# Kernel optimization log

Measured on AMD Instinct MI355X. Metric: run time of the kernel, lower is better.

The kernel has to match this reference:

```python
import jax, jax.numpy as jnp
import numpy as np

B, N, D, H = 4, 2048, 64, 8

def setup_inputs() -> dict:
    key = jax.random.key(0)
    ks = jax.random.split(key, 6)
    s = 0.05
    return {
        "x":  jax.random.normal(ks[0], (B, N, D), dtype=jnp.float32),
        "Wq": jax.random.normal(ks[1], (D, D * H), dtype=jnp.float32) * s,
        "Wk": jax.random.normal(ks[2], (D, D * H), dtype=jnp.float32) * s,
        "Wv": jax.random.normal(ks[3], (D, D * H), dtype=jnp.float32) * s,
        "Wu": jax.random.normal(ks[4], (D * H, D), dtype=jnp.float32) * s,
        "bu": jnp.zeros((D,), dtype=jnp.float32),
    }

def reference(x, Wq, Wk, Wv, Wu, bu):
    b, n, d = x.shape
    h = Wq.shape[1] // d
    # projections: each head has full width d (per the original module)
    q = (x @ Wq).reshape(b, n, h, d).transpose(0, 2, 1, 3)  # [b,h,n,d]
    k = (x @ Wk).reshape(b, n, h, d).transpose(0, 2, 1, 3)
    v = (x @ Wv).reshape(b, n, h, d).transpose(0, 2, 1, 3)
    scores = jnp.einsum('bhnd,bhmd->bhnm', q, k) / jnp.sqrt(jnp.float32(d))
    w = jax.nn.softmax(scores, axis=-1)
    y = jnp.einsum('bhnm,bhmd->bhnd', w, v)          # [b,h,n,d]
    y = y.transpose(0, 2, 1, 3).reshape(b, n, h * d)  # [b,n,h*d]
    return y @ Wu + bu
```

## Files before the change

### kernel.cpp

```cpp
#include <hip/hip_runtime.h>
#include <hip/hip_bf16.h>

#define BB 4
#define NN 2048
#define DD 64
#define HH 8
#define DHH 512

typedef __bf16 bf16_t;
typedef __bf16 bf16x8 __attribute__((ext_vector_type(8)));
typedef __bf16 bf16x4 __attribute__((ext_vector_type(4)));
typedef float f32x4 __attribute__((ext_vector_type(4)));
typedef long long i64;
typedef i64 i64x2 __attribute__((ext_vector_type(2)));
typedef _Float16 f16_t;
typedef _Float16 f16x4 __attribute__((ext_vector_type(4)));
typedef __fp16 h16x2 __attribute__((ext_vector_type(2)));

__device__ __forceinline__ void dma16(const void* g, void* l) {
    __builtin_amdgcn_global_load_lds(
        (const __attribute__((address_space(1))) unsigned int*)g,
        (__attribute__((address_space(3))) unsigned int*)l,
        16, 0, 0);
}

#define MFMA   __builtin_amdgcn_mfma_f32_16x16x32_bf16
#define MFMA8  __builtin_amdgcn_mfma_f32_16x16x32_fp8_fp8
#define MFMA16F __builtin_amdgcn_mfma_f32_16x16x16f16

#define QSCALE 0.18033688011112042f


__global__ __launch_bounds__(256) void prep(
    const float* __restrict__ Wq, const float* __restrict__ Wk,
    const float* __restrict__ Wv, const float* __restrict__ Wu,
    bf16_t* __restrict__ Wqt, bf16_t* __restrict__ Wkt,
    bf16_t* __restrict__ Wvt, bf16_t* __restrict__ Wut)
{
    const int bid = blockIdx.x, tid = threadIdx.x;
    if (bid < 48) {
        const int m = bid >> 4, slice = bid & 15;
        const float* src = (m == 0) ? Wq : (m == 1) ? Wk : Wv;
        bf16_t* dst = (m == 0) ? Wqt : (m == 1) ? Wkt : Wvt;
        const float scale = (m == 0) ? QSCALE : 1.0f;
        const int dc = slice * 32 + (tid >> 3);
        const int kbase = (tid & 7) * 8;
        bf16x8 p;
        #pragma unroll
        for (int j = 0; j < 8; ++j)
            p[j] = (bf16_t)(src[(size_t)(kbase + j) * 512 + dc] * scale);
        *(bf16x8*)(dst + dc * 64 + kbase) = p;
    } else {
        const int kq = (bid - 48) * 32;
        const int dc = tid >> 2, sub = (tid & 3) * 8;
        bf16x8 p;
        #pragma unroll
        for (int j = 0; j < 8; ++j)
            p[j] = (bf16_t)Wu[(size_t)(kq + sub + j) * 64 + dc];
        *(bf16x8*)(Wut + dc * 512 + kq + sub) = p;
    }
}

__global__ __launch_bounds__(256) void qkv_mfma(
    const float* __restrict__ x, const bf16_t* __restrict__ Wqt,
    const bf16_t* __restrict__ Wkt, const bf16_t* __restrict__ Wvt,
    char* __restrict__ q8, char* __restrict__ k8, f16_t* __restrict__ vt)
{
    const int n0   = blockIdx.x * 64;
    const int h    = blockIdx.y;
    const int tid  = threadIdx.x;
    const int w    = tid >> 6;
    const int lane = tid & 63;
    const int quad = lane >> 4;
    const int c    = lane & 15;
    const int cq   = c & 7;
    const int l8   = lane >> 3;
    const int lg   = (lane & 7) ^ l8;
    const int lo   = l8 * 128 + lg * 16;
    const int sw0  = ((quad    ) ^ cq) * 16;
    const int sw1  = ((quad + 4) ^ cq) * 16;
    const int w2048 = w * 2048;

    __shared__ __align__(16) float  xs[64 * 64];
    __shared__ __align__(16) bf16_t Wqs[64 * 64], Wks[64 * 64], Wvs[64 * 64];

    {
        const int rloc = lane >> 4;
        const int s    = lane & 15;
        #pragma unroll
        for (int j = 0; j < 4; ++j) {
            int chunk = w * 4 + j;
            int r7 = (chunk * 4 + rloc) & 7;
            const char* src = (const char*)(x + (size_t)(n0 + chunk * 4 + rloc) * 64)
                            + ((s & 8) | ((s & 7) ^ r7)) * 16;
            dma16(src, (char*)xs + chunk * 1024);
        }
    }
    const char* qg = (const char*)Wqt + (size_t)h * 8192;
    const char* kg = (const char*)Wkt + (size_t)h * 8192;
    const char* vg = (const char*)Wvt + (size_t)h * 8192;
    dma16(qg + w2048 + lo,        (char*)Wqs + w2048);
    dma16(qg + w2048 + 1024 + lo, (char*)Wqs + w2048 + 1024);
    dma16(kg + w2048 + lo,        (char*)Wks + w2048);
    dma16(kg + w2048 + 1024 + lo, (char*)Wks + w2048 + 1024);
    dma16(vg + w2048 + lo,        (char*)Wvs + w2048);
    dma16(vg + w2048 + 1024 + lo, (char*)Wvs + w2048 + 1024);
    __syncthreads();

    auto xfrag = [&](int row, int kk) -> bf16x8 {
        const char* rbase = (const char*)xs + row * 256;
        int g0 = kk * 8 + ((quad * 2    ) ^ cq);
        int g1 = kk * 8 + ((quad * 2 + 1) ^ cq);
        f32x4 a = *(const f32x4*)(rbase + g0 * 16);
        f32x4 b = *(const f32x4*)(rbase + g1 * 16);
        bf16x8 r;
        r[0] = (bf16_t)a[0]; r[1] = (bf16_t)a[1]; r[2] = (bf16_t)a[2]; r[3] = (bf16_t)a[3];
        r[4] = (bf16_t)b[0]; r[5] = (bf16_t)b[1]; r[6] = (bf16_t)b[2]; r[7] = (bf16_t)b[3];
        return r;
    };

    bf16x8 xf0 = xfrag(w * 16 + c, 0);
    bf16x8 xf1 = xfrag(w * 16 + c, 1);

    const int gr = n0 + w * 16 + c;
    const int bb = gr >> 11, nn = gr & 2047;
    char* qrow_g = q8 + (((size_t)bb * HH + h) * NN + nn) * 64;
    char* krow_g = k8 + (((size_t)bb * HH + h) * NN + nn) * 64;
    const int nsw = (nn & 3) ^ ((nn >> 2) & 3);

    #pragma unroll
    for (int mb = 0; mb < 4; ++mb) {
        const char* aq = (const char*)Wqs + (mb * 16 + c) * 128;
        const char* ak = (const char*)Wks + (mb * 16 + c) * 128;
        f32x4 accq = (f32x4){0.f, 0.f, 0.f, 0.f};
        f32x4 acck = (f32x4){0.f, 0.f, 0.f, 0.f};
        accq = MFMA(*(const bf16x8*)(aq + sw0), xf0, accq, 0, 0, 0);
        accq = MFMA(*(const bf16x8*)(aq + sw1), xf1, accq, 0, 0, 0);
        acck = MFMA(*(const bf16x8*)(ak + sw0), xf0, acck, 0, 0, 0);
        acck = MFMA(*(const bf16x8*)(ak + sw1), xf1, acck, 0, 0, 0);
        int g2  = (mb * 2 + (quad >> 1)) & 3;
        int off = ((quad & 1) * 4) + ((mb >> 1) * 8) + ((g2 ^ nsw) * 16);
        int pq = __builtin_amdgcn_cvt_pk_fp8_f32(accq[0], accq[1], 0, false);
        pq     = __builtin_amdgcn_cvt_pk_fp8_f32(accq[2], accq[3], pq, true);
        int pk = __builtin_amdgcn_cvt_pk_fp8_f32(acck[0], acck[1], 0, false);
        pk     = __builtin_amdgcn_cvt_pk_fp8_f32(acck[2], acck[3], pk, true);
        *(int*)(qrow_g + off) = pq;
        *(int*)(krow_g + off) = pk;
    }

    const char* wvrow = (const char*)Wvs + (w * 16 + c) * 128;
    bf16x8 vf0 = *(const bf16x8*)(wvrow + sw0);
    bf16x8 vf1 = *(const bf16x8*)(wvrow + sw1);

    const int bb2 = n0 >> 11;
    f16_t* vtb = vt + ((size_t)bb2 * HH + h) * (size_t)(DD * NN)
               + (size_t)((n0 & 2047) >> 4) * 1024 + quad * 256 + (w * 16 + c) * 4;

    #pragma unroll
    for (int nb = 0; nb < 4; ++nb) {
        f32x4 acc = (f32x4){0.f, 0.f, 0.f, 0.f};
        acc = MFMA(xfrag(nb * 16 + c, 0), vf0, acc, 0, 0, 0);
        acc = MFMA(xfrag(nb * 16 + c, 1), vf1, acc, 0, 0, 0);
        f16x4 p = { (f16_t)acc[0], (f16_t)acc[1], (f16_t)acc[2], (f16_t)acc[3] };
        *(f16x4*)(vtb + nb * 1024) = p;
    }
}

__global__ __launch_bounds__(256, 3) void flash_attn(
    const char* __restrict__ q8, const char* __restrict__ k8,
    const f16_t* __restrict__ vt, bf16_t* __restrict__ y)
{
    const int h    = blockIdx.x;
    const int n0   = blockIdx.y * 64;
    const int b    = blockIdx.z;
    const int tid  = threadIdx.x;
    const int w    = tid >> 6;
    const int lane = tid & 63;
    const int quad = lane >> 4;
    const int c    = lane & 15;
    const int ksw  = (quad ^ (c & 3) ^ ((c >> 2) & 3)) * 16;

    __shared__ __align__(16) char SM[49152];

    const size_t bh = (size_t)(b * HH + h);
    const char* qp = q8 + bh * (size_t)(NN * 64);
    const char* kp = k8 + bh * (size_t)(NN * 64);
    const char* vp = (const char*)(vt + bh * (size_t)(DD * NN));

    i64x2 qf[4];
    #pragma unroll
    for (int cb = 0; cb < 4; ++cb)
        qf[cb] = *(const i64x2*)(qp + (size_t)(n0 + cb * 16 + c) * 64 + ksw);

    const char* kdma = kp + w * 1024 + lane * 16;
    const char* vdma = vp + w * 2048 + lane * 16;

    const int kro = w * 2048 + c * 64 + ksw;
    const int vro = 8192 + w * 4096 + quad * 512 + c * 8;

    f32x4 lsum4[4];
    f32x4 o[4][4];
    #pragma unroll
    for (int cb = 0; cb < 4; ++cb) lsum4[cb] = (f32x4){0.f, 0.f, 0.f, 0.f};
    #pragma unroll
    for (int db = 0; db < 4; ++db)
        #pragma unroll
        for (int cb = 0; cb < 4; ++cb) o[db][cb] = (f32x4){0.f, 0.f, 0.f, 0.f};

    #define STAGE2(p, buf) do {                                               \
        char* B_ = SM + (buf) * 24576;                                        \
        const size_t t0_ = (size_t)(2 * (p));                                 \
        dma16(kdma + t0_ * 4096,         B_ + w * 2048);                      \
        dma16(kdma + t0_ * 4096 + 4096,  B_ + w * 2048 + 1024);               \
        dma16(vdma + t0_ * 8192,         B_ + 8192 + w * 4096);               \
        dma16(vdma + t0_ * 8192 + 1024,  B_ + 8192 + w * 4096 + 1024);        \
        dma16(vdma + t0_ * 8192 + 8192,  B_ + 8192 + w * 4096 + 2048);        \
        dma16(vdma + t0_ * 8192 + 9216,  B_ + 8192 + w * 4096 + 3072);        \
    } while (0)

    #define BODY2(buf, hf) do {                                               \
        const char* kb_b = SM + (buf) * 24576;                                \
        i64x2 kf_ = *(const i64x2*)(kb_b + kro + (hf) * 1024);                \
        f16x4 vf_[4];                                                         \
        _Pragma("unroll")                                                     \
        for (int db = 0; db < 4; ++db)                                        \
            vf_[db] = *(const f16x4*)(kb_b + vro + (hf) * 2048 + db * 128);   \
        _Pragma("unroll")                                                     \
        for (int cb = 0; cb < 4; ++cb) {                                      \
            f32x4 s_ = (f32x4){0.f, 0.f, 0.f, 0.f};                           \
            s_ = MFMA8(kf_.x, qf[cb].x, s_, 0, 0, 0);                         \
            s_ = MFMA8(kf_.y, qf[cb].y, s_, 0, 0, 0);                         \
            float p0_ = __builtin_amdgcn_exp2f(s_[0]);                        \
            float p1_ = __builtin_amdgcn_exp2f(s_[1]);                        \
            float p2_ = __builtin_amdgcn_exp2f(s_[2]);                        \
            float p3_ = __builtin_amdgcn_exp2f(s_[3]);                        \
            lsum4[cb] += (f32x4){p0_, p1_, p2_, p3_};                         \
            h16x2 ab_ = __builtin_amdgcn_cvt_pkrtz(p0_, p1_);                 \
            h16x2 cd_ = __builtin_amdgcn_cvt_pkrtz(p2_, p3_);                 \
            f16x4 pf_;                                                        \
            __builtin_memcpy(&pf_, &ab_, 4);                                  \
            __builtin_memcpy((char*)&pf_ + 4, &cd_, 4);                       \
            _Pragma("unroll")                                                 \
            for (int db = 0; db < 4; ++db)                                    \
                o[db][cb] = MFMA16F(vf_[db], pf_, o[db][cb], 0, 0, 0);        \
        }                                                                     \
    } while (0)

    STAGE2(0, 0);
    asm volatile("s_waitcnt vmcnt(0)" ::: "memory");
    __builtin_amdgcn_sched_barrier(0);
    STAGE2(1, 1);

    #pragma unroll 1
    for (int p = 0; p < 16; ++p) {
        BODY2(p & 1, 0);
        BODY2(p & 1, 1);
        if (p < 15) {
            __builtin_amdgcn_sched_barrier(0);
            if (p < 14) {
                STAGE2(p + 2, p & 1);
                asm volatile("s_waitcnt vmcnt(6)" ::: "memory");
            } else {
                asm volatile("s_waitcnt vmcnt(0)" ::: "memory");
            }
            __builtin_amdgcn_sched_barrier(0);
        }
    }

    #undef STAGE2
    #undef BODY2

    float lsum[4];
    #pragma unroll
    for (int cb = 0; cb < 4; ++cb)
        lsum[cb] = (lsum4[cb][0] + lsum4[cb][1]) + (lsum4[cb][2] + lsum4[cb][3]);

    __syncthreads();

    char*  Ob = SM;
    float* Lb = (float*)(SM + 16384);

    #pragma unroll
    for (int cb = 0; cb < 4; ++cb) {
        lsum[cb] += __shfl_xor(lsum[cb], 16, 64);
        lsum[cb] += __shfl_xor(lsum[cb], 32, 64);
    }
    if (quad == 0) {
        #pragma unroll
        for (int cb = 0; cb < 4; ++cb)
            Lb[(w * 4 + cb) * 16 + c] = lsum[cb];
    }

    #pragma unroll
    for (int ww = 0; ww < 4; ++ww) {
        if (w == ww) {
            #pragma unroll
            for (int db = 0; db < 4; ++db) {
                #pragma unroll
                for (int cb = 0; cb < 4; ++cb) {
                    char* p = Ob + (size_t)(((db * 4 + cb) * 4 + quad) * 16 + c) * 16;
                    f32x4 v = o[db][cb];
                    if (ww > 0) v += *(const f32x4*)p;
                    *(f32x4*)p = v;
                }
            }
        }
        __syncthreads();
    }

    {
        const int n_loc = tid & 63;
        const int dq    = tid >> 6;
        const int qcb   = n_loc >> 4;
        const int cc    = n_loc & 15;
        float l = Lb[(0 * 4 + qcb) * 16 + cc] + Lb[(1 * 4 + qcb) * 16 + cc]
                + Lb[(2 * 4 + qcb) * 16 + cc] + Lb[(3 * 4 + qcb) * 16 + cc];
        float inv = 1.0f / l;
        float vals[16];
        #pragma unroll
        for (int q2 = 0; q2 < 4; ++q2) {
            f32x4 v = *(const f32x4*)(Ob
                    + (size_t)(((dq * 4 + qcb) * 4 + q2) * 16 + cc) * 16);
            vals[q2 * 4 + 0] = v[0]; vals[q2 * 4 + 1] = v[1];
            vals[q2 * 4 + 2] = v[2]; vals[q2 * 4 + 3] = v[3];
        }
        bf16x8 o0, o1;
        #pragma unroll
        for (int j = 0; j < 8; ++j) {
            o0[j] = (bf16_t)(vals[j] * inv);
            o1[j] = (bf16_t)(vals[8 + j] * inv);
        }
        bf16_t* yrow = y + bh * (size_t)(NN * DD) + (size_t)(n0 + n_loc) * DD + dq * 16;
        *(bf16x8*)(yrow)     = o0;
        *(bf16x8*)(yrow + 8) = o1;
    }
}

__global__ __launch_bounds__(256) void out_proj(
    const bf16_t* __restrict__ y,
    const bf16_t* __restrict__ Wut,
    const float* __restrict__ bu, float* __restrict__ out)
{
    const int rt   = blockIdx.x >> 1;
    const int dh   = blockIdx.x & 1;
    const int row0 = rt * 32;
    const int b    = row0 >> 11;
    const int nn0  = row0 & 2047;
    const int tid  = threadIdx.x;
    const int w    = tid >> 6;
    const int lane = tid & 63;
    const int quad = lane >> 4;
    const int c    = lane & 15;
    const int cq   = c & 7;

    __shared__ __align__(16) bf16_t ys[32 * 512];

    {
        const int hsel = lane >> 3;
        const int g7   = lane & 7;
        #pragma unroll
        for (int rr = 0; rr < 8; ++rr) {
            int row = w * 8 + rr;
            const char* src = (const char*)y
                + (((size_t)b * HH + hsel) * NN + nn0 + row) * 128
                + ((g7 ^ (row & 7)) * 16);
            dma16(src, (char*)ys + row * 1024);
        }
    }
    __syncthreads();

    const int rows16 = (w >> 1) * 16;
    const int mb     = dh * 2 + (w & 1);
    const char* yrow = (const char*)ys + (rows16 + c) * 1024;

    f32x4 acc = (f32x4){0.f, 0.f, 0.f, 0.f};
    #pragma unroll
    for (int kk = 0; kk < 16; ++kk) {
        int g = kk * 4 + quad;
        bf16x8 bfrag = *(const bf16x8*)(yrow + (((g & ~7) | ((g & 7) ^ cq)) * 16));
        bf16x8 afrag = *(const bf16x8*)((const char*)Wut
                        + (size_t)(mb * 16 + c) * 1024 + kk * 64 + quad * 16);
        acc = MFMA(afrag, bfrag, acc, 0, 0, 0);
    }

    float4 bb = *(const float4*)(bu + mb * 16 + quad * 4);
    float4 res = { acc[0] + bb.x, acc[1] + bb.y, acc[2] + bb.z, acc[3] + bb.w };
    float* op = out + (size_t)(row0 + rows16 + c) * DD + mb * 16 + quad * 4;
    *(float4*)op = res;
}

extern "C" void kernel_launch(void* const* d_in, const int* in_sizes, int n_in,
                              void* d_out, int out_size, void* d_ws, size_t ws_size,
                              hipStream_t stream) {
    const float* x  = (const float*)d_in[0];
    const float* Wq = (const float*)d_in[1];
    const float* Wk = (const float*)d_in[2];
    const float* Wv = (const float*)d_in[3];
    const float* Wu = (const float*)d_in[4];
    const float* bu = (const float*)d_in[5];
    float* out = (float*)d_out;

    const size_t SEG8 = (size_t)BB * HH * NN * 64;
    const size_t SEG  = SEG8 * 2;
    char* ws = (char*)d_ws;
    char*   q8  = ws;
    char*   k8  = ws + SEG8;
    f16_t*  vt  = (f16_t*)(ws + 2 * SEG8);
    bf16_t* y   = (bf16_t*)(ws + 2 * SEG8 + SEG);
    bf16_t* Wqt = (bf16_t*)(ws + 2 * SEG8 + 2 * SEG);
    bf16_t* Wkt = (bf16_t*)(ws + 2 * SEG8 + 2 * SEG + (1 << 16));
    bf16_t* Wvt = (bf16_t*)(ws + 2 * SEG8 + 2 * SEG + 2 * (1 << 16));
    bf16_t* Wut = (bf16_t*)(ws + 2 * SEG8 + 2 * SEG + 3 * (1 << 16));

    prep<<<dim3(64), dim3(256), 0, stream>>>(Wq, Wk, Wv, Wu, Wqt, Wkt, Wvt, Wut);
    qkv_mfma<<<dim3(128, 8), dim3(256), 0, stream>>>(x, Wqt, Wkt, Wvt, q8, k8, vt);
    flash_attn<<<dim3(HH, NN / 64, BB), dim3(256), 0, stream>>>(q8, k8, vt, y);
    out_proj<<<dim3(512), dim3(256), 0, stream>>>(y, Wut, bu, out);
}
```

Measured before the change: 126.4 us.

## Deepen K/V prefetch pipeline to five single-tile LDS buffers

Replaces the double-buffered two-tile staging with a five-slot ring of single 64-key tiles, keeping four tiles in flight ahead of compute. Each iteration waits only for the oldest outstanding tile, so more global-load latency is hidden. LDS per block grows from 48KB to 60KB and launch bounds drop from three to two blocks per SIMD, which trades occupancy for pipeline depth. The final stage re-fetches tile 31 redundantly to keep the wait count uniform.

```diff
diff --git a/kernel.cpp b/kernel.cpp
--- a/kernel.cpp
+++ b/kernel.cpp
@@ -166,7 +166,7 @@
     }
 }
 
-__global__ __launch_bounds__(256, 3) void flash_attn(
+__global__ __launch_bounds__(256, 2) void flash_attn(
     const char* __restrict__ q8, const char* __restrict__ k8,
     const f16_t* __restrict__ vt, bf16_t* __restrict__ y)
 {
@@ -180,7 +180,7 @@
     const int c    = lane & 15;
     const int ksw  = (quad ^ (c & 3) ^ ((c >> 2) & 3)) * 16;
 
-    __shared__ __align__(16) char SM[49152];
+    __shared__ __align__(16) char SM[61440];
 
     const size_t bh = (size_t)(b * HH + h);
     const char* qp = q8 + bh * (size_t)(NN * 64);
@@ -195,8 +195,8 @@
     const char* kdma = kp + w * 1024 + lane * 16;
     const char* vdma = vp + w * 2048 + lane * 16;
 
-    const int kro = w * 2048 + c * 64 + ksw;
-    const int vro = 8192 + w * 4096 + quad * 512 + c * 8;
+    const int kro = w * 1024 + c * 64 + ksw;
+    const int vro = 4096 + w * 2048 + quad * 512 + c * 8;
 
     f32x4 lsum4[4];
     f32x4 o[4][4];
@@ -207,24 +207,20 @@
         #pragma unroll
         for (int cb = 0; cb < 4; ++cb) o[db][cb] = (f32x4){0.f, 0.f, 0.f, 0.f};
 
-    #define STAGE2(p, buf) do {                                               \
-        char* B_ = SM + (buf) * 24576;                                        \
-        const size_t t0_ = (size_t)(2 * (p));                                 \
-        dma16(kdma + t0_ * 4096,         B_ + w * 2048);                      \
-        dma16(kdma + t0_ * 4096 + 4096,  B_ + w * 2048 + 1024);               \
-        dma16(vdma + t0_ * 8192,         B_ + 8192 + w * 4096);               \
-        dma16(vdma + t0_ * 8192 + 1024,  B_ + 8192 + w * 4096 + 1024);        \
-        dma16(vdma + t0_ * 8192 + 8192,  B_ + 8192 + w * 4096 + 2048);        \
-        dma16(vdma + t0_ * 8192 + 9216,  B_ + 8192 + w * 4096 + 3072);        \
+    #define STAGE1(t, buf) do {                                               \
+        char* B_ = SM + (buf) * 12288;                                        \
+        dma16(kdma + (size_t)(t) * 4096,        B_ + w * 1024);               \
+        dma16(vdma + (size_t)(t) * 8192,        B_ + 4096 + w * 2048);        \
+        dma16(vdma + (size_t)(t) * 8192 + 1024, B_ + 4096 + w * 2048 + 1024); \
     } while (0)
 
-    #define BODY2(buf, hf) do {                                               \
-        const char* kb_b = SM + (buf) * 24576;                                \
-        i64x2 kf_ = *(const i64x2*)(kb_b + kro + (hf) * 1024);                \
+    #define BODY1(buf) do {                                                   \
+        const char* kb_b = SM + (buf) * 12288;                                \
+        i64x2 kf_ = *(const i64x2*)(kb_b + kro);                              \
         f16x4 vf_[4];                                                         \
         _Pragma("unroll")                                                     \
         for (int db = 0; db < 4; ++db)                                        \
-            vf_[db] = *(const f16x4*)(kb_b + vro + (hf) * 2048 + db * 128);   \
+            vf_[db] = *(const f16x4*)(kb_b + vro + db * 128);                 \
         _Pragma("unroll")                                                     \
         for (int cb = 0; cb < 4; ++cb) {                                      \
             f32x4 s_ = (f32x4){0.f, 0.f, 0.f, 0.f};                           \
@@ -246,29 +242,28 @@
         }                                                                     \
     } while (0)
 
-    STAGE2(0, 0);
+    STAGE1(0, 0);
+    STAGE1(1, 1);
+    STAGE1(2, 2);
+    STAGE1(3, 3);
+    asm volatile("s_waitcnt vmcnt(9)" ::: "memory");
+    __builtin_amdgcn_sched_barrier(0);
+
+    #pragma unroll 1
+    for (int t = 0; t < 32; ++t) {
+        BODY1(t % 5);
+        if (t < 31) {
+            __builtin_amdgcn_sched_barrier(0);
+            const int ts = (t + 4 < 32) ? (t + 4) : 31;
+            STAGE1(ts, (t + 4) % 5);
+            asm volatile("s_waitcnt vmcnt(9)" ::: "memory");
+            __builtin_amdgcn_sched_barrier(0);
+        }
+    }
     asm volatile("s_waitcnt vmcnt(0)" ::: "memory");
-    __builtin_amdgcn_sched_barrier(0);
-    STAGE2(1, 1);
-
-    #pragma unroll 1
-    for (int p = 0; p < 16; ++p) {
-        BODY2(p & 1, 0);
-        BODY2(p & 1, 1);
-        if (p < 15) {
-            __builtin_amdgcn_sched_barrier(0);
-            if (p < 14) {
-                STAGE2(p + 2, p & 1);
-                asm volatile("s_waitcnt vmcnt(6)" ::: "memory");
-            } else {
-                asm volatile("s_waitcnt vmcnt(0)" ::: "memory");
-            }
-            __builtin_amdgcn_sched_barrier(0);
-        }
-    }
-
-    #undef STAGE2
-    #undef BODY2
+
+    #undef STAGE1
+    #undef BODY1
 
     float lsum[4];
     #pragma unroll
```

Result: slower. 130.7 us (+3.5%).

## Fuse output projection into flash attention epilogue with atomic accumulation

Applied to the files above, without the earlier changes.

Removes the separate out_proj kernel and the bf16 y intermediate. Each attention block now multiplies its normalized per-head output tile by that head's slice of Wu with MFMA and atomically adds the result into the fp32 output. Head 0 contributes the bias, and the prep kernel zero-fills the output beforehand. This saves a launch and a global round trip for y, but adds contention from eight heads doing fp32 atomics on the same output elements, and the summation order is no longer deterministic.

```diff
diff --git a/kernel.cpp b/kernel.cpp
--- a/kernel.cpp
+++ b/kernel.cpp
@@ -35,9 +35,17 @@
     const float* __restrict__ Wq, const float* __restrict__ Wk,
     const float* __restrict__ Wv, const float* __restrict__ Wu,
     bf16_t* __restrict__ Wqt, bf16_t* __restrict__ Wkt,
-    bf16_t* __restrict__ Wvt, bf16_t* __restrict__ Wut)
+    bf16_t* __restrict__ Wvt, bf16_t* __restrict__ Wut,
+    float* __restrict__ out)
 {
     const int bid = blockIdx.x, tid = threadIdx.x;
+    {
+        float4 z = {0.f, 0.f, 0.f, 0.f};
+        float* op = out + (size_t)bid * 8192 + tid * 4;
+        #pragma unroll
+        for (int i = 0; i < 8; ++i)
+            *(float4*)(op + i * 1024) = z;
+    }
     if (bid < 48) {
         const int m = bid >> 4, slice = bid & 15;
         const float* src = (m == 0) ? Wq : (m == 1) ? Wk : Wv;
@@ -168,7 +176,8 @@
 
 __global__ __launch_bounds__(256, 3) void flash_attn(
     const char* __restrict__ q8, const char* __restrict__ k8,
-    const f16_t* __restrict__ vt, bf16_t* __restrict__ y)
+    const f16_t* __restrict__ vt, const bf16_t* __restrict__ Wut,
+    const float* __restrict__ bu, float* __restrict__ out)
 {
     const int h    = blockIdx.x;
     const int n0   = blockIdx.y * 64;
@@ -309,84 +318,52 @@
     }
 
     {
-        const int n_loc = tid & 63;
-        const int dq    = tid >> 6;
-        const int qcb   = n_loc >> 4;
-        const int cc    = n_loc & 15;
-        float l = Lb[(0 * 4 + qcb) * 16 + cc] + Lb[(1 * 4 + qcb) * 16 + cc]
-                + Lb[(2 * 4 + qcb) * 16 + cc] + Lb[(3 * 4 + qcb) * 16 + cc];
+        float l = Lb[(0 * 4 + w) * 16 + c] + Lb[(1 * 4 + w) * 16 + c]
+                + Lb[(2 * 4 + w) * 16 + c] + Lb[(3 * 4 + w) * 16 + c];
         float inv = 1.0f / l;
-        float vals[16];
-        #pragma unroll
-        for (int q2 = 0; q2 < 4; ++q2) {
-            f32x4 v = *(const f32x4*)(Ob
-                    + (size_t)(((dq * 4 + qcb) * 4 + q2) * 16 + cc) * 16);
-            vals[q2 * 4 + 0] = v[0]; vals[q2 * 4 + 1] = v[1];
-            vals[q2 * 4 + 2] = v[2]; vals[q2 * 4 + 3] = v[3];
-        }
-        bf16x8 o0, o1;
-        #pragma unroll
-        for (int j = 0; j < 8; ++j) {
-            o0[j] = (bf16_t)(vals[j] * inv);
-            o1[j] = (bf16_t)(vals[8 + j] * inv);
-        }
-        bf16_t* yrow = y + bh * (size_t)(NN * DD) + (size_t)(n0 + n_loc) * DD + dq * 16;
-        *(bf16x8*)(yrow)     = o0;
-        *(bf16x8*)(yrow + 8) = o1;
-    }
-}
-
-__global__ __launch_bounds__(256) void out_proj(
-    const bf16_t* __restrict__ y,
-    const bf16_t* __restrict__ Wut,
-    const float* __restrict__ bu, float* __restrict__ out)
-{
-    const int rt   = blockIdx.x >> 1;
-    const int dh   = blockIdx.x & 1;
-    const int row0 = rt * 32;
-    const int b    = row0 >> 11;
-    const int nn0  = row0 & 2047;
-    const int tid  = threadIdx.x;
-    const int w    = tid >> 6;
-    const int lane = tid & 63;
-    const int quad = lane >> 4;
-    const int c    = lane & 15;
-    const int cq   = c & 7;
-
-    __shared__ __align__(16) bf16_t ys[32 * 512];
-
-    {
-        const int hsel = lane >> 3;
-        const int g7   = lane & 7;
-        #pragma unroll
-        for (int rr = 0; rr < 8; ++rr) {
-            int row = w * 8 + rr;
-            const char* src = (const char*)y
-                + (((size_t)b * HH + hsel) * NN + nn0 + row) * 128
-                + ((g7 ^ (row & 7)) * 16);
-            dma16(src, (char*)ys + row * 1024);
-        }
-    }
-    __syncthreads();
-
-    const int rows16 = (w >> 1) * 16;
-    const int mb     = dh * 2 + (w & 1);
-    const char* yrow = (const char*)ys + (rows16 + c) * 1024;
-
-    f32x4 acc = (f32x4){0.f, 0.f, 0.f, 0.f};
-    #pragma unroll
-    for (int kk = 0; kk < 16; ++kk) {
-        int g = kk * 4 + quad;
-        bf16x8 bfrag = *(const bf16x8*)(yrow + (((g & ~7) | ((g & 7) ^ cq)) * 16));
-        bf16x8 afrag = *(const bf16x8*)((const char*)Wut
-                        + (size_t)(mb * 16 + c) * 1024 + kk * 64 + quad * 16);
-        acc = MFMA(afrag, bfrag, acc, 0, 0, 0);
-    }
-
-    float4 bb = *(const float4*)(bu + mb * 16 + quad * 4);
-    float4 res = { acc[0] + bb.x, acc[1] + bb.y, acc[2] + bb.z, acc[3] + bb.w };
-    float* op = out + (size_t)(row0 + rows16 + c) * DD + mb * 16 + quad * 4;
-    *(float4*)op = res;
+
+        f32x4 acc[4];
+        #pragma unroll
+        for (int mb = 0; mb < 4; ++mb) {
+            if (h == 0) {
+                float4 bb4 = *(const float4*)(bu + mb * 16 + quad * 4);
+                acc[mb] = (f32x4){bb4.x, bb4.y, bb4.z, bb4.w};
+            } else {
+                acc[mb] = (f32x4){0.f, 0.f, 0.f, 0.f};
+            }
+        }
+
+        #pragma unroll
+        for (int kk = 0; kk < 2; ++kk) {
+            const int db = kk * 2 + (quad >> 1);
+            const int q0 = (quad & 1) * 2;
+            f32x4 blo = *(const f32x4*)(Ob
+                      + (size_t)(((db * 4 + w) * 4 + q0    ) * 16 + c) * 16);
+            f32x4 bhi = *(const f32x4*)(Ob
+                      + (size_t)(((db * 4 + w) * 4 + q0 + 1) * 16 + c) * 16);
+            bf16x8 bf;
+            bf[0] = (bf16_t)(blo[0] * inv); bf[1] = (bf16_t)(blo[1] * inv);
+            bf[2] = (bf16_t)(blo[2] * inv); bf[3] = (bf16_t)(blo[3] * inv);
+            bf[4] = (bf16_t)(bhi[0] * inv); bf[5] = (bf16_t)(bhi[1] * inv);
+            bf[6] = (bf16_t)(bhi[2] * inv); bf[7] = (bf16_t)(bhi[3] * inv);
+            #pragma unroll
+            for (int mb = 0; mb < 4; ++mb) {
+                bf16x8 af = *(const bf16x8*)((const char*)Wut
+                          + (size_t)(mb * 16 + c) * 1024 + h * 128
+                          + kk * 64 + quad * 16);
+                acc[mb] = MFMA(af, bf, acc[mb], 0, 0, 0);
+            }
+        }
+
+        float* orow = out + ((size_t)b * NN + n0 + w * 16 + c) * DD + quad * 4;
+        #pragma unroll
+        for (int mb = 0; mb < 4; ++mb) {
+            atomicAdd(orow + mb * 16 + 0, acc[mb][0]);
+            atomicAdd(orow + mb * 16 + 1, acc[mb][1]);
+            atomicAdd(orow + mb * 16 + 2, acc[mb][2]);
+            atomicAdd(orow + mb * 16 + 3, acc[mb][3]);
+        }
+    }
 }
 
 extern "C" void kernel_launch(void* const* d_in, const int* in_sizes, int n_in,
@@ -406,14 +383,12 @@
     char*   q8  = ws;
     char*   k8  = ws + SEG8;
     f16_t*  vt  = (f16_t*)(ws + 2 * SEG8);
-    bf16_t* y   = (bf16_t*)(ws + 2 * SEG8 + SEG);
     bf16_t* Wqt = (bf16_t*)(ws + 2 * SEG8 + 2 * SEG);
     bf16_t* Wkt = (bf16_t*)(ws + 2 * SEG8 + 2 * SEG + (1 << 16));
     bf16_t* Wvt = (bf16_t*)(ws + 2 * SEG8 + 2 * SEG + 2 * (1 << 16));
     bf16_t* Wut = (bf16_t*)(ws + 2 * SEG8 + 2 * SEG + 3 * (1 << 16));
 
-    prep<<<dim3(64), dim3(256), 0, stream>>>(Wq, Wk, Wv, Wu, Wqt, Wkt, Wvt, Wut);
+    prep<<<dim3(64), dim3(256), 0, stream>>>(Wq, Wk, Wv, Wu, Wqt, Wkt, Wvt, Wut, out);
     qkv_mfma<<<dim3(128, 8), dim3(256), 0, stream>>>(x, Wqt, Wkt, Wvt, q8, k8, vt);
-    flash_attn<<<dim3(HH, NN / 64, BB), dim3(256), 0, stream>>>(q8, k8, vt, y);
-    out_proj<<<dim3(512), dim3(256), 0, stream>>>(y, Wut, bu, out);
-}
+    flash_attn<<<dim3(HH, NN / 64, BB), dim3(256), 0, stream>>>(q8, k8, vt, Wut, bu, out);
+}
```

Result: slower. 150.4 us (+19.0%).

## Fold weight prep kernel into QKV projection, staging fp32 weights directly

Applied to the files above, without the earlier changes.

Removes the separate prep launch. The QKV kernel now DMAs the fp32 Wq/Wk/Wv head slices straight into LDS and converts them to bf16 (with the Q scale applied) while building MFMA fragments. The Wu transpose is done by a subset of blocks at the end of the QKV kernel. This saves one kernel launch and one global round-trip for the converted weights. In exchange it adds extra LDS traffic, strided scalar LDS reads, a second staging pass with two more barriers for Wv, and redundant conversion work repeated in every block.

```diff
diff --git a/kernel.cpp b/kernel.cpp
--- a/kernel.cpp
+++ b/kernel.cpp
@@ -9,7 +9,6 @@
 
 typedef __bf16 bf16_t;
 typedef __bf16 bf16x8 __attribute__((ext_vector_type(8)));
-typedef __bf16 bf16x4 __attribute__((ext_vector_type(4)));
 typedef float f32x4 __attribute__((ext_vector_type(4)));
 typedef long long i64;
 typedef i64 i64x2 __attribute__((ext_vector_type(2)));
@@ -31,40 +30,12 @@
 #define QSCALE 0.18033688011112042f
 
 
-__global__ __launch_bounds__(256) void prep(
+__global__ __launch_bounds__(256) void qkv_mfma(
+    const float* __restrict__ x,
     const float* __restrict__ Wq, const float* __restrict__ Wk,
     const float* __restrict__ Wv, const float* __restrict__ Wu,
-    bf16_t* __restrict__ Wqt, bf16_t* __restrict__ Wkt,
-    bf16_t* __restrict__ Wvt, bf16_t* __restrict__ Wut)
-{
-    const int bid = blockIdx.x, tid = threadIdx.x;
-    if (bid < 48) {
-        const int m = bid >> 4, slice = bid & 15;
-        const float* src = (m == 0) ? Wq : (m == 1) ? Wk : Wv;
-        bf16_t* dst = (m == 0) ? Wqt : (m == 1) ? Wkt : Wvt;
-        const float scale = (m == 0) ? QSCALE : 1.0f;
-        const int dc = slice * 32 + (tid >> 3);
-        const int kbase = (tid & 7) * 8;
-        bf16x8 p;
-        #pragma unroll
-        for (int j = 0; j < 8; ++j)
-            p[j] = (bf16_t)(src[(size_t)(kbase + j) * 512 + dc] * scale);
-        *(bf16x8*)(dst + dc * 64 + kbase) = p;
-    } else {
-        const int kq = (bid - 48) * 32;
-        const int dc = tid >> 2, sub = (tid & 3) * 8;
-        bf16x8 p;
-        #pragma unroll
-        for (int j = 0; j < 8; ++j)
-            p[j] = (bf16_t)Wu[(size_t)(kq + sub + j) * 64 + dc];
-        *(bf16x8*)(Wut + dc * 512 + kq + sub) = p;
-    }
-}
-
-__global__ __launch_bounds__(256) void qkv_mfma(
-    const float* __restrict__ x, const bf16_t* __restrict__ Wqt,
-    const bf16_t* __restrict__ Wkt, const bf16_t* __restrict__ Wvt,
-    char* __restrict__ q8, char* __restrict__ k8, f16_t* __restrict__ vt)
+    char* __restrict__ q8, char* __restrict__ k8, f16_t* __restrict__ vt,
+    bf16_t* __restrict__ Wut)
 {
     const int n0   = blockIdx.x * 64;
     const int h    = blockIdx.y;
@@ -74,15 +45,10 @@
     const int quad = lane >> 4;
     const int c    = lane & 15;
     const int cq   = c & 7;
-    const int l8   = lane >> 3;
-    const int lg   = (lane & 7) ^ l8;
-    const int lo   = l8 * 128 + lg * 16;
-    const int sw0  = ((quad    ) ^ cq) * 16;
-    const int sw1  = ((quad + 4) ^ cq) * 16;
-    const int w2048 = w * 2048;
-
-    __shared__ __align__(16) float  xs[64 * 64];
-    __shared__ __align__(16) bf16_t Wqs[64 * 64], Wks[64 * 64], Wvs[64 * 64];
+
+    __shared__ __align__(16) float xs[64 * 64];
+    __shared__ __align__(16) float WA[64 * 64];
+    __shared__ __align__(16) float WB[64 * 64];
 
     {
         const int rloc = lane >> 4;
@@ -96,15 +62,19 @@
             dma16(src, (char*)xs + chunk * 1024);
         }
     }
-    const char* qg = (const char*)Wqt + (size_t)h * 8192;
-    const char* kg = (const char*)Wkt + (size_t)h * 8192;
-    const char* vg = (const char*)Wvt + (size_t)h * 8192;
-    dma16(qg + w2048 + lo,        (char*)Wqs + w2048);
-    dma16(qg + w2048 + 1024 + lo, (char*)Wqs + w2048 + 1024);
-    dma16(kg + w2048 + lo,        (char*)Wks + w2048);
-    dma16(kg + w2048 + 1024 + lo, (char*)Wks + w2048 + 1024);
-    dma16(vg + w2048 + lo,        (char*)Wvs + w2048);
-    dma16(vg + w2048 + 1024 + lo, (char*)Wvs + w2048 + 1024);
+    const int rsub = lane >> 4;
+    const int gcol = (lane & 15) * 16;
+    #define WSTAGE(SRC, DST) do {                                             \
+        _Pragma("unroll")                                                     \
+        for (int j_ = 0; j_ < 4; ++j_) {                                      \
+            const int r_ = w * 16 + j_ * 4;                                   \
+            dma16((const char*)(SRC) + (size_t)(r_ + rsub) * 2048             \
+                      + (size_t)h * 256 + gcol,                               \
+                  (char*)(DST) + r_ * 256);                                   \
+        }                                                                     \
+    } while (0)
+    WSTAGE(Wq, WA);
+    WSTAGE(Wk, WB);
     __syncthreads();
 
     auto xfrag = [&](int row, int kk) -> bf16x8 {
@@ -118,9 +88,19 @@
         r[4] = (bf16_t)b[0]; r[5] = (bf16_t)b[1]; r[6] = (bf16_t)b[2]; r[7] = (bf16_t)b[3];
         return r;
     };
+    auto wfrag = [&](const float* base, int dc, int k0, float scale) -> bf16x8 {
+        const float* p = base + k0 * 64 + dc;
+        bf16x8 r;
+        #pragma unroll
+        for (int j = 0; j < 8; ++j)
+            r[j] = (bf16_t)(p[j * 64] * scale);
+        return r;
+    };
 
     bf16x8 xf0 = xfrag(w * 16 + c, 0);
     bf16x8 xf1 = xfrag(w * 16 + c, 1);
+    const int k0a = quad * 8;
+    const int k0b = 32 + quad * 8;
 
     const int gr = n0 + w * 16 + c;
     const int bb = gr >> 11, nn = gr & 2047;
@@ -130,14 +110,13 @@
 
     #pragma unroll
     for (int mb = 0; mb < 4; ++mb) {
-        const char* aq = (const char*)Wqs + (mb * 16 + c) * 128;
-        const char* ak = (const char*)Wks + (mb * 16 + c) * 128;
+        const int dc = mb * 16 + c;
         f32x4 accq = (f32x4){0.f, 0.f, 0.f, 0.f};
         f32x4 acck = (f32x4){0.f, 0.f, 0.f, 0.f};
-        accq = MFMA(*(const bf16x8*)(aq + sw0), xf0, accq, 0, 0, 0);
-        accq = MFMA(*(const bf16x8*)(aq + sw1), xf1, accq, 0, 0, 0);
-        acck = MFMA(*(const bf16x8*)(ak + sw0), xf0, acck, 0, 0, 0);
-        acck = MFMA(*(const bf16x8*)(ak + sw1), xf1, acck, 0, 0, 0);
+        accq = MFMA(wfrag(WA, dc, k0a, QSCALE), xf0, accq, 0, 0, 0);
+        accq = MFMA(wfrag(WA, dc, k0b, QSCALE), xf1, accq, 0, 0, 0);
+        acck = MFMA(wfrag(WB, dc, k0a, 1.0f),  xf0, acck, 0, 0, 0);
+        acck = MFMA(wfrag(WB, dc, k0b, 1.0f),  xf1, acck, 0, 0, 0);
         int g2  = (mb * 2 + (quad >> 1)) & 3;
         int off = ((quad & 1) * 4) + ((mb >> 1) * 8) + ((g2 ^ nsw) * 16);
         int pq = __builtin_amdgcn_cvt_pk_fp8_f32(accq[0], accq[1], 0, false);
@@ -148,9 +127,13 @@
         *(int*)(krow_g + off) = pk;
     }
 
-    const char* wvrow = (const char*)Wvs + (w * 16 + c) * 128;
-    bf16x8 vf0 = *(const bf16x8*)(wvrow + sw0);
-    bf16x8 vf1 = *(const bf16x8*)(wvrow + sw1);
+    __syncthreads();
+    WSTAGE(Wv, WA);
+    __syncthreads();
+    #undef WSTAGE
+
+    bf16x8 vf0 = wfrag(WA, w * 16 + c, k0a, 1.0f);
+    bf16x8 vf1 = wfrag(WA, w * 16 + c, k0b, 1.0f);
 
     const int bb2 = n0 >> 11;
     f16_t* vtb = vt + ((size_t)bb2 * HH + h) * (size_t)(DD * NN)
@@ -163,6 +146,16 @@
         acc = MFMA(xfrag(nb * 16 + c, 1), vf1, acc, 0, 0, 0);
         f16x4 p = { (f16_t)acc[0], (f16_t)acc[1], (f16_t)acc[2], (f16_t)acc[3] };
         *(f16x4*)(vtb + nb * 1024) = p;
+    }
+
+    if (h == 7 && blockIdx.x < 16) {
+        const int kq = blockIdx.x * 32;
+        const int dc = tid >> 2, sub = (tid & 3) * 8;
+        bf16x8 p;
+        #pragma unroll
+        for (int j = 0; j < 8; ++j)
+            p[j] = (bf16_t)Wu[(size_t)(kq + sub + j) * 64 + dc];
+        *(bf16x8*)(Wut + dc * 512 + kq + sub) = p;
     }
 }
 
@@ -407,13 +400,10 @@
     char*   k8  = ws + SEG8;
     f16_t*  vt  = (f16_t*)(ws + 2 * SEG8);
     bf16_t* y   = (bf16_t*)(ws + 2 * SEG8 + SEG);
-    bf16_t* Wqt = (bf16_t*)(ws + 2 * SEG8 + 2 * SEG);
-    bf16_t* Wkt = (bf16_t*)(ws + 2 * SEG8 + 2 * SEG + (1 << 16));
-    bf16_t* Wvt = (bf16_t*)(ws + 2 * SEG8 + 2 * SEG + 2 * (1 << 16));
-    bf16_t* Wut = (bf16_t*)(ws + 2 * SEG8 + 2 * SEG + 3 * (1 << 16));
-
-    prep<<<dim3(64), dim3(256), 0, stream>>>(Wq, Wk, Wv, Wu, Wqt, Wkt, Wvt, Wut);
-    qkv_mfma<<<dim3(128, 8), dim3(256), 0, stream>>>(x, Wqt, Wkt, Wvt, q8, k8, vt);
+    bf16_t* Wut = (bf16_t*)(ws + 2 * SEG8 + 2 * SEG);
+
+    qkv_mfma<<<dim3(128, 8), dim3(256), 0, stream>>>(x, Wq, Wk, Wv, Wu,
+                                                     q8, k8, vt, Wut);
     flash_attn<<<dim3(HH, NN / 64, BB), dim3(256), 0, stream>>>(q8, k8, vt, y);
     out_proj<<<dim3(512), dim3(256), 0, stream>>>(y, Wut, bu, out);
 }
```

New measurement: 126.7 us. Within noise of the previous version (+0.3%).
